# Kernel tuning notes

Measured on AMD Instinct MI355X. Metric: run time of the kernel, lower is better.

## Reference

```python
import jax, jax.numpy as jnp
import numpy as np

EMB = 1024
HEADS = 16
DEPTH = EMB // HEADS
B, S = 8, 1024


def setup_inputs() -> dict:
    key = jax.random.key(0)
    ks = jax.random.split(key, 12)
    sc = 0.02
    return {
        "q": jax.random.normal(ks[0], (B, S, EMB), jnp.float32),
        "k": jax.random.normal(ks[1], (B, S, EMB), jnp.float32),
        "v": jax.random.normal(ks[2], (B, S, EMB), jnp.float32),
        # per-head Dense weights stacked: [H, EMB, DEPTH], biases [H, DEPTH]
        "Wq": jax.random.normal(ks[3], (HEADS, EMB, DEPTH), jnp.float32) * sc,
        "bq": jnp.zeros((HEADS, DEPTH), jnp.float32),
        "Wk": jax.random.normal(ks[4], (HEADS, EMB, DEPTH), jnp.float32) * sc,
        "bk": jnp.zeros((HEADS, DEPTH), jnp.float32),
        "Wv": jax.random.normal(ks[5], (HEADS, EMB, DEPTH), jnp.float32) * sc,
        "bv": jnp.zeros((HEADS, DEPTH), jnp.float32),
        # output Dense: [EMB, EMB], bias [EMB]
        "Wo": jax.random.normal(ks[6], (EMB, EMB), jnp.float32) * sc,
        "bo": jnp.zeros((EMB,), jnp.float32),
    }


def reference(q, k, v, Wq, bq, Wk, bk, Wv, bv, Wo, bo):
    # Per-head Dense projections, batched over heads via einsum.
    # qh: [B, H, S, DEPTH]
    qh = jnp.einsum("bsd,hde->bhse", q, Wq) + bq[None, :, None, :]
    kh = jnp.einsum("bsd,hde->bhse", k, Wk) + bk[None, :, None, :]
    vh = jnp.einsum("bsd,hde->bhse", v, Wv) + bv[None, :, None, :]
    # Scaled dot-product attention per head: logits [B, H, Sq, Sk]
    scale = 1.0 / jnp.sqrt(jnp.asarray(DEPTH, jnp.float32))
    logits = jnp.einsum("bhqe,bhke->bhqk", qh, kh) * scale
    attn = jax.nn.softmax(logits, axis=-1)
    ctx = jnp.einsum("bhqk,bhke->bhqe", attn, vh)  # [B, H, S, DEPTH]
    # concat heads along last axis (head order preserved)
    ctx = jnp.transpose(ctx, (0, 2, 1, 3)).reshape(B, S, EMB)
    return ctx @ Wo + bo
```

## Files before the change

### kernel.cpp

```cpp
#include <hip/hip_runtime.h>
#include <hip/hip_bf16.h>
#include <stdint.h>

typedef __bf16 bf16;
typedef __attribute__((ext_vector_type(8))) __bf16 bf16x8;
typedef __attribute__((ext_vector_type(4))) __bf16 bf16x4;
typedef __attribute__((ext_vector_type(4))) float f32x4;

#define GLD(g, l) __builtin_amdgcn_global_load_lds( \
    (const __attribute__((address_space(1))) void*)(g), \
    (__attribute__((address_space(3))) void*)(l), 16, 0, 0)

__device__ __forceinline__ f32x4 mfma16(bf16x8 a, bf16x8 b, f32x4 c) {
  return __builtin_amdgcn_mfma_f32_16x16x32_bf16(a, b, c, 0, 0, 0);
}
__device__ __forceinline__ float fexp2(float x) {
  return __builtin_amdgcn_exp2f(x);
}
__device__ __forceinline__ bf16x8 cvt8(const float4& a, const float4& b) {
  bf16x8 p;
  p[0] = (bf16)a.x; p[1] = (bf16)a.y; p[2] = (bf16)a.z; p[3] = (bf16)a.w;
  p[4] = (bf16)b.x; p[5] = (bf16)b.y; p[6] = (bf16)b.z; p[7] = (bf16)b.w;
  return p;
}

__device__ __forceinline__ void compute128(const bf16* buf, int wr, int wc,
                                           int lr, int quad,
                                           f32x4 (&acc)[4][4]) {
  bf16x8 af[4], bfr[4];
#pragma unroll
  for (int i = 0; i < 4; i++) {
    const int ra = wr + i * 16 + lr;
    const int rb = wc + i * 16 + lr;
    af[i]  = *(const bf16x8*)(buf + ra * 32 + ((quad ^ ((ra >> 1) & 3)) * 8));
    bfr[i] = *(const bf16x8*)(buf + 4096 + rb * 32 +
                              ((quad ^ ((rb >> 1) & 3)) * 8));
  }
  __builtin_amdgcn_s_setprio(1);
#pragma unroll
  for (int im = 0; im < 4; im++)
#pragma unroll
    for (int in = 0; in < 4; in++)
      acc[im][in] = mfma16(af[im], bfr[in], acc[im][in]);
  __builtin_amdgcn_s_setprio(0);
}

#define WAIT_BAR(cnt)                                            \
  asm volatile("s_waitcnt vmcnt(" #cnt ")" ::: "memory");        \
  __builtin_amdgcn_s_barrier();                                  \
  asm volatile("" ::: "memory")

__global__ void wtrans3(const float* __restrict__ Wq, const float* __restrict__ Wk,
                        const float* __restrict__ Wv, bf16* __restrict__ WT)
{
  __shared__ bf16 t[32][33];
  const int w = blockIdx.z;
  const float* W = (w == 0) ? Wq : (w == 1) ? Wk : Wv;
  const int h = blockIdx.x >> 1;
  const int c0 = (blockIdx.x & 1) * 32;
  const int r0 = blockIdx.y * 32;
  const float* s = W + (size_t)h * 65536;
  bf16* d = WT + (size_t)w * (1 << 20) + (size_t)h * 65536;
  const int tx = threadIdx.x, ty = threadIdx.y;
#pragma unroll
  for (int i = 0; i < 32; i += 8)
    t[ty + i][tx] = (bf16)s[(r0 + ty + i) * 64 + c0 + tx];
  __syncthreads();
#pragma unroll
  for (int i = 0; i < 32; i += 8)
    d[(c0 + ty + i) * 1024 + r0 + tx] = t[tx][ty + i];
}

__global__ void wtransO(const float* __restrict__ src, bf16* __restrict__ dst)
{
  __shared__ bf16 t[32][33];
  const int c0 = blockIdx.x * 32, r0 = blockIdx.y * 32;
  const int tx = threadIdx.x, ty = threadIdx.y;
#pragma unroll
  for (int i = 0; i < 32; i += 8)
    t[ty + i][tx] = (bf16)src[(r0 + ty + i) * 1024 + c0 + tx];
  __syncthreads();
#pragma unroll
  for (int i = 0; i < 32; i += 8)
    dst[(c0 + ty + i) * 1024 + r0 + tx] = t[tx][ty + i];
}

__global__ __launch_bounds__(256) void cast2(const float* __restrict__ q,
                                             const float* __restrict__ k,
                                             bf16* __restrict__ qc,
                                             bf16* __restrict__ kc)
{
  const float* s = blockIdx.y ? k : q;
  bf16* d = blockIdx.y ? kc : qc;
  const size_t i = ((size_t)blockIdx.x * 256 + threadIdx.x) * 8;
  float4 a = *(const float4*)(s + i);
  float4 b = *(const float4*)(s + i + 4);
  *(bf16x8*)(d + i) = cvt8(a, b);
}

__global__ __launch_bounds__(256) void proj_qkv(
    const bf16* __restrict__ qc, const bf16* __restrict__ kc,
    const float* __restrict__ v, const bf16* __restrict__ WT,
    const float* __restrict__ bq, const float* __restrict__ bk,
    const float* __restrict__ bv, bf16* __restrict__ qh,
    bf16* __restrict__ kh, bf16* __restrict__ vt, float cscale)
{
  __shared__ bf16 S[24576];
  const int tid = threadIdx.x;
  const int wave = tid >> 6, lane = tid & 63;
  const int lr = lane & 15, quad = lane >> 4;
  const int n0 = blockIdx.x * 128;
  const int mt = blockIdx.y;
  const int mseg = mt * 128;
  const int seg = mseg >> 13;
  const int m0 = mseg & 8191;
  const int wr = (wave >> 1) * 64, wc = (wave & 1) * 64;

  const float* bias = (seg == 0) ? bq : (seg == 1) ? bk : bv;
  const bf16* Bt = WT + (size_t)seg * (1 << 20);

  f32x4 acc[4][4];
#pragma unroll
  for (int i = 0; i < 4; i++)
#pragma unroll
    for (int j = 0; j < 4; j++)
#pragma unroll
      for (int e = 0; e < 4; e++) acc[i][j][e] = 0.f;

  const int srow = tid >> 2;
  const int sko = ((tid & 3) ^ ((srow >> 1) & 3)) * 8;
  const bf16* bPtr = Bt + (size_t)(n0 + srow) * 1024 + sko;

  int i0 = 0, i1 = 1, i2 = 2;

  if (seg < 2) {
    const bf16* Ab = (seg == 1) ? kc : qc;
    const bf16* aPtr = Ab + (size_t)(m0 + srow) * 1024 + sko;
#pragma unroll
    for (int t = 0; t < 2; ++t) {
      bf16* nb = S + t * 8192;
      GLD(aPtr + t * 32,             nb + tid * 8);
      GLD(aPtr + 64 * 1024 + t * 32, nb + 2048 + tid * 8);
      GLD(bPtr + t * 32,             nb + 4096 + tid * 8);
      GLD(bPtr + 64 * 1024 + t * 32, nb + 6144 + tid * 8);
    }
    for (int it = 0; it < 30; ++it) {
      WAIT_BAR(4);
      const int k0 = (it + 2) * 32;
      bf16* nb = S + i2 * 8192;
      GLD(aPtr + k0,             nb + tid * 8);
      GLD(aPtr + 64 * 1024 + k0, nb + 2048 + tid * 8);
      GLD(bPtr + k0,             nb + 4096 + tid * 8);
      GLD(bPtr + 64 * 1024 + k0, nb + 6144 + tid * 8);
      compute128(S + i0 * 8192, wr, wc, lr, quad, acc);
      const int t = i0; i0 = i1; i1 = i2; i2 = t;
    }
    WAIT_BAR(4);
    compute128(S + i0 * 8192, wr, wc, lr, quad, acc);
    WAIT_BAR(0);
    compute128(S + i1 * 8192, wr, wc, lr, quad, acc);
  } else {
    const int ar = tid >> 1, acb = (tid & 1) * 2;
    const int asw = (ar >> 1) & 3;
    const float* vPtr = v + (size_t)(m0 + ar) * 1024 + acb * 8;
    float4 f[4];
#pragma unroll
    for (int j = 0; j < 4; j++) f[j] = *(const float4*)(vPtr + j * 4);
    {
      *(bf16x8*)(S + ar * 32 + ((acb ^ asw) * 8))       = cvt8(f[0], f[1]);
      *(bf16x8*)(S + ar * 32 + (((acb + 1) ^ asw) * 8)) = cvt8(f[2], f[3]);
    }
    GLD(bPtr,                  S + 4096 + tid * 8);
    GLD(bPtr + 64 * 1024,      S + 6144 + tid * 8);
    GLD(bPtr + 32,             S + 8192 + 4096 + tid * 8);
    GLD(bPtr + 64 * 1024 + 32, S + 8192 + 6144 + tid * 8);
    asm volatile("s_waitcnt vmcnt(2)" ::: "memory");
    for (int it = 0; it < 32; ++it) {
      asm volatile("s_waitcnt lgkmcnt(0)" ::: "memory");
      __builtin_amdgcn_sched_barrier(0);
      __builtin_amdgcn_s_barrier();
      asm volatile("" ::: "memory");
      const bool moreA = (it + 1 < 32);
      if (moreA) {
        const int k0 = (it + 1) * 32;
#pragma unroll
        for (int j = 0; j < 4; j++) f[j] = *(const float4*)(vPtr + k0 + j * 4);
      }
      if (it + 2 < 32) {
        const int k0 = (it + 2) * 32;
        bf16* nb = S + i2 * 8192;
        GLD(bPtr + k0,             nb + 4096 + tid * 8);
        GLD(bPtr + 64 * 1024 + k0, nb + 6144 + tid * 8);
      }
      compute128(S + i0 * 8192, wr, wc, lr, quad, acc);
      if (moreA) {
        bf16* nb = S + i1 * 8192;
        *(bf16x8*)(nb + ar * 32 + ((acb ^ asw) * 8))       = cvt8(f[0], f[1]);
        *(bf16x8*)(nb + ar * 32 + (((acb + 1) ^ asw) * 8)) = cvt8(f[2], f[3]);
      }
      const int t = i0; i0 = i1; i1 = i2; i2 = t;
    }
  }

  const int qd = quad * 4;
  float bv4[4];
#pragma unroll
  for (int in = 0; in < 4; in++) bv4[in] = bias[n0 + wc + in * 16 + lr];

  if (seg < 2) {
    bf16* C = (seg == 0) ? qh : kh;
    const float cmul = (seg == 0) ? cscale : 1.0f;
#pragma unroll
    for (int im = 0; im < 4; im++) {
      const int row = m0 + wr + im * 16 + qd;
#pragma unroll
      for (int in = 0; in < 4; in++) {
        const int col = n0 + wc + in * 16 + lr;
#pragma unroll
        for (int i = 0; i < 4; i++)
          C[(size_t)(row + i) * 1024 + col] = (bf16)((acc[im][in][i] + bv4[in]) * cmul);
      }
    }
  } else {
#pragma unroll
    for (int im = 0; im < 4; im++) {
      const int row = m0 + wr + im * 16 + qd;
      const int b = row >> 10, sin = row & 1023;
#pragma unroll
      for (int in = 0; in < 4; in++) {
        const int col = n0 + wc + in * 16 + lr;
        const int h = col >> 6, e = col & 63;
        bf16x4 pk;
#pragma unroll
        for (int i = 0; i < 4; i++) pk[i] = (bf16)(acc[im][in][i] + bv4[in]);
        *(bf16x4*)(vt + (size_t)(b * 16 + h) * 65536 + e * 1024 + sin) = pk;
      }
    }
  }
}

__global__ __launch_bounds__(256) void gemm_a16_c32(
    const bf16* __restrict__ A, const bf16* __restrict__ Bt,
    const float* __restrict__ bias, float* __restrict__ C)
{
  __shared__ bf16 S[24576];
  const int tid = threadIdx.x;
  const int wave = tid >> 6, lane = tid & 63;
  const int lr = lane & 15, quad = lane >> 4;
  const int n0 = blockIdx.x * 128;
  const int m0 = blockIdx.y * 128;
  const int wr = (wave >> 1) * 64, wc = (wave & 1) * 64;

  f32x4 acc[4][4];
#pragma unroll
  for (int i = 0; i < 4; i++)
#pragma unroll
    for (int j = 0; j < 4; j++)
#pragma unroll
      for (int e = 0; e < 4; e++) acc[i][j][e] = 0.f;

  const int srow = tid >> 2;
  const int sko = ((tid & 3) ^ ((srow >> 1) & 3)) * 8;
  const bf16* aPtr = A + (size_t)(m0 + srow) * 1024 + sko;
  const bf16* bPtr = Bt + (size_t)(n0 + srow) * 1024 + sko;

  int i0 = 0, i1 = 1, i2 = 2;
#pragma unroll
  for (int t = 0; t < 2; ++t) {
    bf16* nb = S + t * 8192;
    GLD(aPtr + t * 32,             nb + tid * 8);
    GLD(aPtr + 64 * 1024 + t * 32, nb + 2048 + tid * 8);
    GLD(bPtr + t * 32,             nb + 4096 + tid * 8);
    GLD(bPtr + 64 * 1024 + t * 32, nb + 6144 + tid * 8);
  }
  for (int it = 0; it < 30; ++it) {
    WAIT_BAR(4);
    const int k0 = (it + 2) * 32;
    bf16* nb = S + i2 * 8192;
    GLD(aPtr + k0,             nb + tid * 8);
    GLD(aPtr + 64 * 1024 + k0, nb + 2048 + tid * 8);
    GLD(bPtr + k0,             nb + 4096 + tid * 8);
    GLD(bPtr + 64 * 1024 + k0, nb + 6144 + tid * 8);
    compute128(S + i0 * 8192, wr, wc, lr, quad, acc);
    const int t = i0; i0 = i1; i1 = i2; i2 = t;
  }
  WAIT_BAR(4);
  compute128(S + i0 * 8192, wr, wc, lr, quad, acc);
  WAIT_BAR(0);
  compute128(S + i1 * 8192, wr, wc, lr, quad, acc);

  const int qd = quad * 4;
  float bv4[4];
#pragma unroll
  for (int in = 0; in < 4; in++) bv4[in] = bias[n0 + wc + in * 16 + lr];
#pragma unroll
  for (int im = 0; im < 4; im++) {
    const int row = m0 + wr + im * 16 + qd;
#pragma unroll
    for (int in = 0; in < 4; in++) {
      const int col = n0 + wc + in * 16 + lr;
#pragma unroll
      for (int i = 0; i < 4; i++)
        C[(size_t)(row + i) * 1024 + col] = acc[im][in][i] + bv4[in];
    }
  }
}

__global__ __launch_bounds__(256) void attn_k(
    const bf16* Q, const bf16* __restrict__ Kh,
    const bf16* __restrict__ Vt, bf16* O)
{
  __shared__ bf16 sK[64 * 72];
  __shared__ bf16 sV[64 * 72];
  __shared__ bf16 sP[128 * 72];
  const int h = blockIdx.x, b = blockIdx.y, q0 = blockIdx.z * 128;
  const int tid = threadIdx.x, wave = tid >> 6, lane = tid & 63;
  const int lr = lane & 15, quad = lane >> 4, kq = quad * 8;
  const int wq = wave * 32;

  const bf16* Qb = Q + (size_t)(b * 1024 + q0) * 1024 + h * 64;
  const bf16* Kb = Kh + (size_t)(b * 1024) * 1024 + h * 64;
  const bf16* Vb = Vt + (size_t)(b * 16 + h) * 65536;

  bf16x8 qf[2][2];
#pragma unroll
  for (int rg = 0; rg < 2; rg++)
#pragma unroll
    for (int ks = 0; ks < 2; ks++)
      qf[rg][ks] = *(const bf16x8*)(Qb + (wq + rg * 16 + lr) * 1024 + ks * 32 + kq);

  f32x4 o[2][4];
  float rsum[2][4];
#pragma unroll
  for (int rg = 0; rg < 2; rg++) {
#pragma unroll
    for (int et = 0; et < 4; et++)
#pragma unroll
      for (int e = 0; e < 4; e++) o[rg][et][e] = 0.f;
#pragma unroll
    for (int i = 0; i < 4; i++) rsum[rg][i] = 0.f;
  }

  const int r = tid >> 3;
  const int c = (tid & 7) * 8;

  bf16x8 k1 = *(const bf16x8*)(Kb + (size_t)r * 1024 + c);
  bf16x8 k2 = *(const bf16x8*)(Kb + (size_t)(32 + r) * 1024 + c);
  bf16x8 v1 = *(const bf16x8*)(Vb + (size_t)r * 1024 + c);
  bf16x8 v2 = *(const bf16x8*)(Vb + (size_t)(32 + r) * 1024 + c);

  for (int kv0 = 0; kv0 < 1024; kv0 += 64) {
    __syncthreads();
    *(bf16x8*)(sK + r * 72 + c) = k1;
    *(bf16x8*)(sK + (32 + r) * 72 + c) = k2;
    *(bf16x8*)(sV + r * 72 + c) = v1;
    *(bf16x8*)(sV + (32 + r) * 72 + c) = v2;
    __syncthreads();
    if (kv0 + 64 < 1024) {
      k1 = *(const bf16x8*)(Kb + (size_t)(kv0 + 64 + r) * 1024 + c);
      k2 = *(const bf16x8*)(Kb + (size_t)(kv0 + 96 + r) * 1024 + c);
      v1 = *(const bf16x8*)(Vb + (size_t)r * 1024 + kv0 + 64 + c);
      v2 = *(const bf16x8*)(Vb + (size_t)(32 + r) * 1024 + kv0 + 64 + c);
    }

    f32x4 sc[2][4];
#pragma unroll
    for (int nt = 0; nt < 4; nt++) {
      bf16x8 kf0 = *(const bf16x8*)(sK + (nt * 16 + lr) * 72 + kq);
      bf16x8 kf1 = *(const bf16x8*)(sK + (nt * 16 + lr) * 72 + 32 + kq);
#pragma unroll
      for (int rg = 0; rg < 2; rg++) {
        f32x4 z;
#pragma unroll
        for (int e = 0; e < 4; e++) z[e] = 0.f;
        z = mfma16(qf[rg][0], kf0, z);
        z = mfma16(qf[rg][1], kf1, z);
        sc[rg][nt] = z;
      }
    }

#pragma unroll
    for (int rg = 0; rg < 2; rg++)
#pragma unroll
      for (int i = 0; i < 4; i++) {
        float p0 = fexp2(sc[rg][0][i]);
        float p1 = fexp2(sc[rg][1][i]);
        float p2 = fexp2(sc[rg][2][i]);
        float p3 = fexp2(sc[rg][3][i]);
        rsum[rg][i] += (p0 + p1) + (p2 + p3);
        const int prow = (wq + rg * 16 + quad * 4 + i) * 72;
        sP[prow + 0 * 16 + lr] = (bf16)p0;
        sP[prow + 1 * 16 + lr] = (bf16)p1;
        sP[prow + 2 * 16 + lr] = (bf16)p2;
        sP[prow + 3 * 16 + lr] = (bf16)p3;
      }
    __syncthreads();

#pragma unroll
    for (int et = 0; et < 4; et++) {
      bf16x8 vf0 = *(const bf16x8*)(sV + (et * 16 + lr) * 72 + kq);
      bf16x8 vf1 = *(const bf16x8*)(sV + (et * 16 + lr) * 72 + 32 + kq);
#pragma unroll
      for (int rg = 0; rg < 2; rg++) {
        bf16x8 pa = *(const bf16x8*)(sP + (wq + rg * 16 + lr) * 72 + kq);
        bf16x8 pb = *(const bf16x8*)(sP + (wq + rg * 16 + lr) * 72 + 32 + kq);
        o[rg][et] = mfma16(pa, vf0, o[rg][et]);
        o[rg][et] = mfma16(pb, vf1, o[rg][et]);
      }
    }
  }

#pragma unroll
  for (int rg = 0; rg < 2; rg++)
#pragma unroll
    for (int i = 0; i < 4; i++) {
      float rs = rsum[rg][i];
#pragma unroll
      for (int off = 1; off < 16; off <<= 1)
        rs += __shfl_xor(rs, off, 64);
      rsum[rg][i] = 1.f / rs;
    }

  bf16* Ob = O + (size_t)(b * 1024 + q0) * 1024 + h * 64;
#pragma unroll
  for (int rg = 0; rg < 2; rg++)
#pragma unroll
    for (int i = 0; i < 4; i++) {
      const int row = wq + rg * 16 + quad * 4 + i;
#pragma unroll
      for (int et = 0; et < 4; et++)
        Ob[row * 1024 + et * 16 + lr] = (bf16)(o[rg][et][i] * rsum[rg][i]);
    }
}

extern "C" void kernel_launch(void* const* d_in, const int* in_sizes, int n_in,
                              void* d_out, int out_size, void* d_ws, size_t ws_size,
                              hipStream_t stream)
{
  const float* q  = (const float*)d_in[0];
  const float* k  = (const float*)d_in[1];
  const float* v  = (const float*)d_in[2];
  const float* Wq = (const float*)d_in[3];
  const float* bq = (const float*)d_in[4];
  const float* Wk = (const float*)d_in[5];
  const float* bk = (const float*)d_in[6];
  const float* Wv = (const float*)d_in[7];
  const float* bv = (const float*)d_in[8];
  const float* Wo = (const float*)d_in[9];
  const float* bo = (const float*)d_in[10];
  float* out = (float*)d_out;
  bf16* ws = (bf16*)d_ws;

  const int MB = 1 << 20;
  bf16* WT  = ws;
  bf16* qh  = ws + 3 * MB;
  bf16* kh  = ws + 11 * MB;
  bf16* vt  = ws + 19 * MB;
  bf16* WoT = ws + 27 * MB;
  bf16* qc  = (bf16*)d_out;
  bf16* kc  = (bf16*)d_out + 8 * MB;

  const float cscale = 0.1803368801111601f;

  dim3 tb(32, 8);
  wtrans3<<<dim3(32, 32, 3), tb, 0, stream>>>(Wq, Wk, Wv, WT);
  wtransO<<<dim3(32, 32), tb, 0, stream>>>(Wo, WoT);
  cast2<<<dim3(4096, 2), 256, 0, stream>>>(q, k, qc, kc);

  proj_qkv<<<dim3(8, 192), 256, 0, stream>>>(qc, kc, v, WT, bq, bk, bv,
                                             qh, kh, vt, cscale);

  attn_k<<<dim3(16, 8, 8), 256, 0, stream>>>(qh, kh, vt, qh);

  gemm_a16_c32<<<dim3(8, 64), 256, 0, stream>>>(qh, WoT, bo, out);
}
```

Baseline: 328.4 us.

## Fuse fp32 casting into QKV projection, merge weight transposes, reorder attention grid

Drops the separate cast kernel for q and k. All three projection segments now read fp32 activations directly and convert them to bf16 in registers before storing to LDS, the path previously used only for v. The two weight-transpose kernels are merged into one launch. The attention grid is reordered so consecutive blocks share a head and batch, and MFMA sections get raised wave priority. This removes a full fp32-to-bf16 round trip through memory and two launches, but the q/k projection loses its async global-to-LDS A loads.

```diff
diff --git a/kernel.cpp b/kernel.cpp
--- a/kernel.cpp
+++ b/kernel.cpp
@@ -50,56 +50,41 @@
   __builtin_amdgcn_s_barrier();                                  \
   asm volatile("" ::: "memory")
 
-__global__ void wtrans3(const float* __restrict__ Wq, const float* __restrict__ Wk,
-                        const float* __restrict__ Wv, bf16* __restrict__ WT)
+__global__ void wtransA(const float* __restrict__ Wq, const float* __restrict__ Wk,
+                        const float* __restrict__ Wv, const float* __restrict__ Wo,
+                        bf16* __restrict__ WT, bf16* __restrict__ WoT)
 {
   __shared__ bf16 t[32][33];
   const int w = blockIdx.z;
-  const float* W = (w == 0) ? Wq : (w == 1) ? Wk : Wv;
-  const int h = blockIdx.x >> 1;
-  const int c0 = (blockIdx.x & 1) * 32;
-  const int r0 = blockIdx.y * 32;
-  const float* s = W + (size_t)h * 65536;
-  bf16* d = WT + (size_t)w * (1 << 20) + (size_t)h * 65536;
   const int tx = threadIdx.x, ty = threadIdx.y;
-#pragma unroll
-  for (int i = 0; i < 32; i += 8)
-    t[ty + i][tx] = (bf16)s[(r0 + ty + i) * 64 + c0 + tx];
-  __syncthreads();
-#pragma unroll
-  for (int i = 0; i < 32; i += 8)
-    d[(c0 + ty + i) * 1024 + r0 + tx] = t[tx][ty + i];
-}
-
-__global__ void wtransO(const float* __restrict__ src, bf16* __restrict__ dst)
-{
-  __shared__ bf16 t[32][33];
-  const int c0 = blockIdx.x * 32, r0 = blockIdx.y * 32;
-  const int tx = threadIdx.x, ty = threadIdx.y;
-#pragma unroll
-  for (int i = 0; i < 32; i += 8)
-    t[ty + i][tx] = (bf16)src[(r0 + ty + i) * 1024 + c0 + tx];
-  __syncthreads();
-#pragma unroll
-  for (int i = 0; i < 32; i += 8)
-    dst[(c0 + ty + i) * 1024 + r0 + tx] = t[tx][ty + i];
-}
-
-__global__ __launch_bounds__(256) void cast2(const float* __restrict__ q,
-                                             const float* __restrict__ k,
-                                             bf16* __restrict__ qc,
-                                             bf16* __restrict__ kc)
-{
-  const float* s = blockIdx.y ? k : q;
-  bf16* d = blockIdx.y ? kc : qc;
-  const size_t i = ((size_t)blockIdx.x * 256 + threadIdx.x) * 8;
-  float4 a = *(const float4*)(s + i);
-  float4 b = *(const float4*)(s + i + 4);
-  *(bf16x8*)(d + i) = cvt8(a, b);
+  if (w < 3) {
+    const float* W = (w == 0) ? Wq : (w == 1) ? Wk : Wv;
+    const int h = blockIdx.x >> 1;
+    const int c0 = (blockIdx.x & 1) * 32;
+    const int r0 = blockIdx.y * 32;
+    const float* s = W + (size_t)h * 65536;
+    bf16* d = WT + (size_t)w * (1 << 20) + (size_t)h * 65536;
+#pragma unroll
+    for (int i = 0; i < 32; i += 8)
+      t[ty + i][tx] = (bf16)s[(r0 + ty + i) * 64 + c0 + tx];
+    __syncthreads();
+#pragma unroll
+    for (int i = 0; i < 32; i += 8)
+      d[(c0 + ty + i) * 1024 + r0 + tx] = t[tx][ty + i];
+  } else {
+    const int c0 = blockIdx.x * 32, r0 = blockIdx.y * 32;
+#pragma unroll
+    for (int i = 0; i < 32; i += 8)
+      t[ty + i][tx] = (bf16)Wo[(r0 + ty + i) * 1024 + c0 + tx];
+    __syncthreads();
+#pragma unroll
+    for (int i = 0; i < 32; i += 8)
+      WoT[(c0 + ty + i) * 1024 + r0 + tx] = t[tx][ty + i];
+  }
 }
 
 __global__ __launch_bounds__(256) void proj_qkv(
-    const bf16* __restrict__ qc, const bf16* __restrict__ kc,
+    const float* __restrict__ q, const float* __restrict__ k,
     const float* __restrict__ v, const bf16* __restrict__ WT,
     const float* __restrict__ bq, const float* __restrict__ bk,
     const float* __restrict__ bv, bf16* __restrict__ qh,
@@ -116,6 +101,7 @@
   const int m0 = mseg & 8191;
   const int wr = (wave >> 1) * 64, wc = (wave & 1) * 64;
 
+  const float* Asrc = (seg == 0) ? q : (seg == 1) ? k : v;
   const float* bias = (seg == 0) ? bq : (seg == 1) ? bk : bv;
   const bf16* Bt = WT + (size_t)seg * (1 << 20);
 
@@ -131,75 +117,48 @@
   const int sko = ((tid & 3) ^ ((srow >> 1) & 3)) * 8;
   const bf16* bPtr = Bt + (size_t)(n0 + srow) * 1024 + sko;
 
+  const int ar = tid >> 1, acb = (tid & 1) * 2;
+  const int asw = (ar >> 1) & 3;
+  const float* aPtr = Asrc + (size_t)(m0 + ar) * 1024 + acb * 8;
+
   int i0 = 0, i1 = 1, i2 = 2;
 
-  if (seg < 2) {
-    const bf16* Ab = (seg == 1) ? kc : qc;
-    const bf16* aPtr = Ab + (size_t)(m0 + srow) * 1024 + sko;
-#pragma unroll
-    for (int t = 0; t < 2; ++t) {
-      bf16* nb = S + t * 8192;
-      GLD(aPtr + t * 32,             nb + tid * 8);
-      GLD(aPtr + 64 * 1024 + t * 32, nb + 2048 + tid * 8);
-      GLD(bPtr + t * 32,             nb + 4096 + tid * 8);
-      GLD(bPtr + 64 * 1024 + t * 32, nb + 6144 + tid * 8);
-    }
-    for (int it = 0; it < 30; ++it) {
-      WAIT_BAR(4);
+  float4 f[4];
+#pragma unroll
+  for (int j = 0; j < 4; j++) f[j] = *(const float4*)(aPtr + j * 4);
+  {
+    *(bf16x8*)(S + ar * 32 + ((acb ^ asw) * 8))       = cvt8(f[0], f[1]);
+    *(bf16x8*)(S + ar * 32 + (((acb + 1) ^ asw) * 8)) = cvt8(f[2], f[3]);
+  }
+  GLD(bPtr,                  S + 4096 + tid * 8);
+  GLD(bPtr + 64 * 1024,      S + 6144 + tid * 8);
+  GLD(bPtr + 32,             S + 8192 + 4096 + tid * 8);
+  GLD(bPtr + 64 * 1024 + 32, S + 8192 + 6144 + tid * 8);
+  asm volatile("s_waitcnt vmcnt(2)" ::: "memory");
+  for (int it = 0; it < 32; ++it) {
+    asm volatile("s_waitcnt lgkmcnt(0)" ::: "memory");
+    __builtin_amdgcn_sched_barrier(0);
+    __builtin_amdgcn_s_barrier();
+    asm volatile("" ::: "memory");
+    const bool moreA = (it + 1 < 32);
+    if (moreA) {
+      const int k0 = (it + 1) * 32;
+#pragma unroll
+      for (int j = 0; j < 4; j++) f[j] = *(const float4*)(aPtr + k0 + j * 4);
+    }
+    if (it + 2 < 32) {
       const int k0 = (it + 2) * 32;
       bf16* nb = S + i2 * 8192;
-      GLD(aPtr + k0,             nb + tid * 8);
-      GLD(aPtr + 64 * 1024 + k0, nb + 2048 + tid * 8);
       GLD(bPtr + k0,             nb + 4096 + tid * 8);
       GLD(bPtr + 64 * 1024 + k0, nb + 6144 + tid * 8);
-      compute128(S + i0 * 8192, wr, wc, lr, quad, acc);
-      const int t = i0; i0 = i1; i1 = i2; i2 = t;
-    }
-    WAIT_BAR(4);
+    }
     compute128(S + i0 * 8192, wr, wc, lr, quad, acc);
-    WAIT_BAR(0);
-    compute128(S + i1 * 8192, wr, wc, lr, quad, acc);
-  } else {
-    const int ar = tid >> 1, acb = (tid & 1) * 2;
-    const int asw = (ar >> 1) & 3;
-    const float* vPtr = v + (size_t)(m0 + ar) * 1024 + acb * 8;
-    float4 f[4];
-#pragma unroll
-    for (int j = 0; j < 4; j++) f[j] = *(const float4*)(vPtr + j * 4);
-    {
-      *(bf16x8*)(S + ar * 32 + ((acb ^ asw) * 8))       = cvt8(f[0], f[1]);
-      *(bf16x8*)(S + ar * 32 + (((acb + 1) ^ asw) * 8)) = cvt8(f[2], f[3]);
-    }
-    GLD(bPtr,                  S + 4096 + tid * 8);
-    GLD(bPtr + 64 * 1024,      S + 6144 + tid * 8);
-    GLD(bPtr + 32,             S + 8192 + 4096 + tid * 8);
-    GLD(bPtr + 64 * 1024 + 32, S + 8192 + 6144 + tid * 8);
-    asm volatile("s_waitcnt vmcnt(2)" ::: "memory");
-    for (int it = 0; it < 32; ++it) {
-      asm volatile("s_waitcnt lgkmcnt(0)" ::: "memory");
-      __builtin_amdgcn_sched_barrier(0);
-      __builtin_amdgcn_s_barrier();
-      asm volatile("" ::: "memory");
-      const bool moreA = (it + 1 < 32);
-      if (moreA) {
-        const int k0 = (it + 1) * 32;
-#pragma unroll
-        for (int j = 0; j < 4; j++) f[j] = *(const float4*)(vPtr + k0 + j * 4);
-      }
-      if (it + 2 < 32) {
-        const int k0 = (it + 2) * 32;
-        bf16* nb = S + i2 * 8192;
-        GLD(bPtr + k0,             nb + 4096 + tid * 8);
-        GLD(bPtr + 64 * 1024 + k0, nb + 6144 + tid * 8);
-      }
-      compute128(S + i0 * 8192, wr, wc, lr, quad, acc);
-      if (moreA) {
-        bf16* nb = S + i1 * 8192;
-        *(bf16x8*)(nb + ar * 32 + ((acb ^ asw) * 8))       = cvt8(f[0], f[1]);
-        *(bf16x8*)(nb + ar * 32 + (((acb + 1) ^ asw) * 8)) = cvt8(f[2], f[3]);
-      }
-      const int t = i0; i0 = i1; i1 = i2; i2 = t;
-    }
+    if (moreA) {
+      bf16* nb = S + i1 * 8192;
+      *(bf16x8*)(nb + ar * 32 + ((acb ^ asw) * 8))       = cvt8(f[0], f[1]);
+      *(bf16x8*)(nb + ar * 32 + (((acb + 1) ^ asw) * 8)) = cvt8(f[2], f[3]);
+    }
+    const int t = i0; i0 = i1; i1 = i2; i2 = t;
   }
 
   const int qd = quad * 4;
@@ -313,7 +272,7 @@
   __shared__ bf16 sK[64 * 72];
   __shared__ bf16 sV[64 * 72];
   __shared__ bf16 sP[128 * 72];
-  const int h = blockIdx.x, b = blockIdx.y, q0 = blockIdx.z * 128;
+  const int q0 = blockIdx.x * 128, h = blockIdx.y, b = blockIdx.z;
   const int tid = threadIdx.x, wave = tid >> 6, lane = tid & 63;
   const int lr = lane & 15, quad = lane >> 4, kq = quad * 8;
   const int wq = wave * 32;
@@ -364,6 +323,7 @@
     }
 
     f32x4 sc[2][4];
+    __builtin_amdgcn_s_setprio(1);
 #pragma unroll
     for (int nt = 0; nt < 4; nt++) {
       bf16x8 kf0 = *(const bf16x8*)(sK + (nt * 16 + lr) * 72 + kq);
@@ -378,6 +338,7 @@
         sc[rg][nt] = z;
       }
     }
+    __builtin_amdgcn_s_setprio(0);
 
 #pragma unroll
     for (int rg = 0; rg < 2; rg++)
@@ -396,6 +357,7 @@
       }
     __syncthreads();
 
+    __builtin_amdgcn_s_setprio(1);
 #pragma unroll
     for (int et = 0; et < 4; et++) {
       bf16x8 vf0 = *(const bf16x8*)(sV + (et * 16 + lr) * 72 + kq);
@@ -408,6 +370,7 @@
         o[rg][et] = mfma16(pb, vf1, o[rg][et]);
       }
     }
+    __builtin_amdgcn_s_setprio(0);
   }
 
 #pragma unroll
@@ -457,20 +420,16 @@
   bf16* kh  = ws + 11 * MB;
   bf16* vt  = ws + 19 * MB;
   bf16* WoT = ws + 27 * MB;
-  bf16* qc  = (bf16*)d_out;
-  bf16* kc  = (bf16*)d_out + 8 * MB;
 
   const float cscale = 0.1803368801111601f;
 
   dim3 tb(32, 8);
-  wtrans3<<<dim3(32, 32, 3), tb, 0, stream>>>(Wq, Wk, Wv, WT);
-  wtransO<<<dim3(32, 32), tb, 0, stream>>>(Wo, WoT);
-  cast2<<<dim3(4096, 2), 256, 0, stream>>>(q, k, qc, kc);
-
-  proj_qkv<<<dim3(8, 192), 256, 0, stream>>>(qc, kc, v, WT, bq, bk, bv,
+  wtransA<<<dim3(32, 32, 4), tb, 0, stream>>>(Wq, Wk, Wv, Wo, WT, WoT);
+
+  proj_qkv<<<dim3(8, 192), 256, 0, stream>>>(q, k, v, WT, bq, bk, bv,
                                              qh, kh, vt, cscale);
 
-  attn_k<<<dim3(16, 8, 8), 256, 0, stream>>>(qh, kh, vt, qh);
+  attn_k<<<dim3(8, 16, 8), 256, 0, stream>>>(qh, kh, vt, qh);
 
   gemm_a16_c32<<<dim3(8, 64), 256, 0, stream>>>(qh, WoT, bo, out);
 }
```

Measured after the change: 345.7 us. 1.05x slower.
